# Performance work log

Hardware: AMD Instinct MI355X
Metric: run time of the kernel (lower is better)

Reference implementation:

```python
import jax, jax.numpy as jnp
import numpy as np

B, CIN, H, W = 4, 64, 160, 160
G, K = 8, 3
KK = K * K
PAD = K // 2
CG = CIN // G  # channels per deformable group


def setup_inputs() -> dict:
    key = jax.random.key(0)
    ks = jax.random.split(key, 6)
    x = jax.random.normal(ks[0], (B, CIN, H, W), jnp.float32)
    feat = jax.random.normal(ks[1], (B, CIN, H, W), jnp.float32)
    # conv_offset weights (zero-init in the original; small random here so offsets are nontrivial)
    w_off = jax.random.normal(ks[2], (3 * G * KK, CIN, 3, 3), jnp.float32) * 0.01
    b_off = jax.random.normal(ks[3], (3 * G * KK,), jnp.float32) * 0.01
    # deformable conv weights (torchvision DeformConv2d: groups=1, bias=True)
    w_dcn = jax.random.normal(ks[4], (CIN, CIN, K, K), jnp.float32) * (1.0 / np.sqrt(CIN * KK))
    b_dcn = jax.random.normal(ks[5], (CIN,), jnp.float32) * 0.01
    return dict(x=x, feat=feat, w_off=w_off, b_off=b_off, w_dcn=w_dcn, b_dcn=b_dcn)


def _modulated_deform_conv(x, offset, mask, w, b):
    # x: [B,C,H,W]; offset: [B,2*G*KK,H,W] (interleaved dy,dx per (g,k));
    # mask: [B,G*KK,H,W]; w: [Cout,C,K,K]; stride 1, zero padding K//2.
    Bn, C, Hh, Ww = x.shape
    off = offset.reshape(Bn, G, KK, 2, Hh, Ww)
    dy = off[:, :, :, 0]  # [B,G,KK,H,W]
    dx = off[:, :, :, 1]
    ki = jnp.arange(K)
    base_y = (jnp.repeat(ki, K) - PAD).reshape(1, 1, KK, 1, 1).astype(x.dtype)
    base_x = (jnp.tile(ki, K) - PAD).reshape(1, 1, KK, 1, 1).astype(x.dtype)
    hy = jnp.arange(Hh, dtype=x.dtype).reshape(1, 1, 1, Hh, 1)
    wx = jnp.arange(Ww, dtype=x.dtype).reshape(1, 1, 1, 1, Ww)
    py = hy + base_y + dy  # sample rows  [B,G,KK,H,W]
    px = wx + base_x + dx  # sample cols
    y0 = jnp.floor(py)
    x0 = jnp.floor(px)
    ly = py - y0
    lx = px - x0
    y0i = y0.astype(jnp.int32)
    x0i = x0.astype(jnp.int32)
    xg = x.reshape(Bn, G, CG, Hh * Ww)

    def gather(yi, xi):
        valid = ((yi >= 0) & (yi < Hh) & (xi >= 0) & (xi < Ww)).astype(x.dtype)
        idx = jnp.clip(yi, 0, Hh - 1) * Ww + jnp.clip(xi, 0, Ww - 1)
        flat = idx.reshape(Bn, G, 1, KK * Hh * Ww)
        v = jnp.take_along_axis(xg, flat, axis=3).reshape(Bn, G, CG, KK, Hh, Ww)
        return v * valid[:, :, None]  # zero padding outside

    v = ((1 - ly) * (1 - lx))[:, :, None] * gather(y0i, x0i) \
      + ((1 - ly) * lx)[:, :, None] * gather(y0i, x0i + 1) \
      + (ly * (1 - lx))[:, :, None] * gather(y0i + 1, x0i) \
      + (ly * lx)[:, :, None] * gather(y0i + 1, x0i + 1)
    v = v * mask.reshape(Bn, G, 1, KK, Hh, Ww)
    wr = w.reshape(w.shape[0], G, CG, KK)
    out = jnp.einsum('ogck,bgckhw->bohw', wr, v) + b[None, :, None, None]
    return out


def reference(x, feat, w_off, b_off, w_dcn, b_dcn):
    # conv_offset: 3x3 conv, stride 1, pad 1
    out = jax.lax.conv_general_dilated(
        feat, w_off, (1, 1), ((1, 1), (1, 1)),
        dimension_numbers=('NCHW', 'OIHW', 'NCHW')) + b_off[None, :, None, None]
    o1, o2, m = jnp.split(out, 3, axis=1)
    offset = jnp.concatenate([o1, o2], axis=1)  # [B, 2*G*KK, H, W]
    mask = jax.nn.sigmoid(m)                    # [B, G*KK, H, W]
    return _modulated_deform_conv(x, offset, mask, w_dcn, b_dcn)
```

## Files before the change

### kernel.cpp

```cpp
#include <hip/hip_runtime.h>
#include <math.h>

#define Bn   4
#define CINc 64
#define Hh   160
#define Ww   160
#define Gg   8
#define HW   (Hh * Ww)
#define COFF 216

#define VROW 200
#define SMEM_U32 7040
#define MASKL_OFF_U16 9344

typedef short bf16x8 __attribute__((ext_vector_type(8)));
typedef float f32x4  __attribute__((ext_vector_type(4)));

static __device__ __forceinline__ unsigned short f2bf(float f) {
    unsigned int u = __float_as_uint(f);
    u = (u + 0x7fffu + ((u >> 16) & 1u)) >> 16;
    return (unsigned short)u;
}
static __device__ __forceinline__ float bf2f(unsigned short s) {
    return __uint_as_float(((unsigned int)s) << 16);
}
static __device__ __forceinline__ float blo(unsigned int u) {
    return __uint_as_float(u << 16);
}
static __device__ __forceinline__ float bhi(unsigned int u) {
    return __uint_as_float(u & 0xffff0000u);
}

__global__ __launch_bounds__(256)
void prep_kernel(const float* __restrict__ feat, const float* __restrict__ x,
                 const float* __restrict__ w_off, const float* __restrict__ w_dcn,
                 unsigned short* __restrict__ featT, unsigned short* __restrict__ xG,
                 unsigned short* __restrict__ wofrag, unsigned short* __restrict__ wfrag) {
    const int blk = blockIdx.x;
    const int t = threadIdx.x;
    if (blk < 800) {
        const int b  = blk / 200;
        const int q  = (blk % 200) * 32 + (t >> 3);
        const int cj = t & 7;
        const float* fb = feat + (size_t)b * CINc * HW;
        float4 v[8];
        #pragma unroll
        for (int m = 0; m < 8; ++m)
            v[m] = *(const float4*)(fb + (size_t)(cj * 8 + m) * HW + q * 4);
        uint4* dst = (uint4*)featT + ((size_t)b * HW + q * 4) * 8 + cj;
        #pragma unroll
        for (int k = 0; k < 4; ++k) {
            float e[8];
            #pragma unroll
            for (int m = 0; m < 8; ++m) {
                const float4 vv = v[m];
                e[m] = (k == 0) ? vv.x : (k == 1) ? vv.y : (k == 2) ? vv.z : vv.w;
            }
            unsigned int d0, d1, d2, d3;
            asm("v_cvt_pk_bf16_f32 %0, %1, %2" : "=v"(d0) : "v"(e[0]), "v"(e[1]));
            asm("v_cvt_pk_bf16_f32 %0, %1, %2" : "=v"(d1) : "v"(e[2]), "v"(e[3]));
            asm("v_cvt_pk_bf16_f32 %0, %1, %2" : "=v"(d2) : "v"(e[4]), "v"(e[5]));
            asm("v_cvt_pk_bf16_f32 %0, %1, %2" : "=v"(d3) : "v"(e[6]), "v"(e[7]));
            uint4 r4; r4.x = d0; r4.y = d1; r4.z = d2; r4.w = d3;
            dst[(size_t)k * 8] = r4;
        }
    } else if (blk < 1600) {
        const int r  = blk - 800;
        const int bg = r / 25;
        const int q  = (r % 25) * 256 + t;
        const float* xb = x + ((size_t)(bg >> 3) * CINc + (size_t)(bg & 7) * 8) * HW;
        float4 v[8];
        #pragma unroll
        for (int cg = 0; cg < 8; ++cg)
            v[cg] = *(const float4*)(xb + (size_t)cg * HW + q * 4);
        uint4* dst = (uint4*)xG + (size_t)bg * HW + q * 4;
        #pragma unroll
        for (int k = 0; k < 4; ++k) {
            float e[8];
            #pragma unroll
            for (int cg = 0; cg < 8; ++cg) {
                const float4 vv = v[cg];
                e[cg] = (k == 0) ? vv.x : (k == 1) ? vv.y : (k == 2) ? vv.z : vv.w;
            }
            unsigned int d0, d1, d2, d3;
            asm("v_cvt_pk_bf16_f32 %0, %1, %2" : "=v"(d0) : "v"(e[0]), "v"(e[1]));
            asm("v_cvt_pk_bf16_f32 %0, %1, %2" : "=v"(d1) : "v"(e[2]), "v"(e[3]));
            asm("v_cvt_pk_bf16_f32 %0, %1, %2" : "=v"(d2) : "v"(e[4]), "v"(e[5]));
            asm("v_cvt_pk_bf16_f32 %0, %1, %2" : "=v"(d3) : "v"(e[6]), "v"(e[7]));
            uint4 r4; r4.x = d0; r4.y = d1; r4.z = d2; r4.w = d3;
            dst[k] = r4;
        }
    } else {
        for (int e = (blk - 1600) * 256 + t; e < 147456 + 36864; e += 180 * 256) {
            if (e < 147456) {
                const int j    = e & 7;
                const int lane = (e >> 3) & 63;
                const int rest = e >> 9;
                const int mt = rest & 15;
                const int q  = rest >> 4;
                const int ks = q & 1;
                const int kp = q >> 1;
                const int co = mt * 16 + (lane & 15);
                const int ci = ks * 32 + (lane >> 4) * 8 + j;
                float v = (co < COFF) ? w_off[(size_t)co * 576 + ci * 9 + kp] : 0.f;
                wofrag[e] = f2bf(v);
            } else {
                const int e2   = e - 147456;
                const int j    = e2 & 7;
                const int lane = (e2 >> 3) & 63;
                const int mt   = (e2 >> 9) & 3;
                const int ks   = e2 >> 11;
                const int m = mt * 16 + (lane & 15);
                const int k = ks * 32 + (lane >> 4) * 8 + j;
                const int g = k / 72, r = k % 72;
                const int kk = r >> 3, cg = r & 7;
                const int ci = g * 8 + cg;
                wfrag[e2] = f2bf(w_dcn[((size_t)m * CINc + ci) * 9 + kk]);
            }
        }
    }
}

#define BLEND_J(out_, w00, w01, w10, w11, c00, c01, c10, c11) {            \
    float vl_ = (c00) * blo(w00) + (c01) * blo(w01)                        \
              + (c10) * blo(w10) + (c11) * blo(w11);                       \
    float vh_ = (c00) * bhi(w00) + (c01) * bhi(w01)                        \
              + (c10) * bhi(w10) + (c11) * bhi(w11);                       \
    asm("v_cvt_pk_bf16_f32 %0, %1, %2" : "=v"(out_) : "v"(vl_), "v"(vh_)); \
}

__global__ __launch_bounds__(256, 4)
void dcnpack_fused(const unsigned short* __restrict__ featT,
                   const unsigned short* __restrict__ xG,
                   const unsigned short* __restrict__ wofrag,
                   const unsigned short* __restrict__ wfrag,
                   const float* __restrict__ b_off,
                   const float* __restrict__ b_dcn,
                   float* __restrict__ out) {
    __shared__ unsigned int smem4[SMEM_U32];
    unsigned short* halo   = (unsigned short*)smem4;
    unsigned int*   offsYX = smem4;
    unsigned short* maskL  = (unsigned short*)smem4 + MASKL_OFF_U16;
    unsigned short* vbuf   = (unsigned short*)smem4;

    const int b  = blockIdx.z;
    const int h0 = blockIdx.y * 8;
    const int w0 = blockIdx.x * 8;
    const int t  = threadIdx.x;
    const int wv   = t >> 6;
    const int lane = t & 63;
    const int n    = lane & 15;
    const int kg   = lane >> 4;

    for (int task = t; task < 800; task += 256) {
        const int pix = task >> 3, ch = task & 7;
        const int ry = pix / 10, rx = pix % 10;
        const int gh = h0 - 1 + ry, gw = w0 - 1 + rx;
        float4 v = make_float4(0.f, 0.f, 0.f, 0.f);
        if (gh >= 0 && gh < Hh && gw >= 0 && gw < Ww)
            v = *(const float4*)(featT + ((((size_t)b * Hh) + gh) * Ww + gw) * CINc + ch * 8);
        *(float4*)(halo + pix * 72 + ch * 8) = v;
    }
    __syncthreads();

    const int bbase0 = (((n >> 3) * 10) + (n & 7)) * 72 + kg * 8;

    f32x4 cacc[4][4] = {};
    bf16x8 af[3][4];
    #pragma unroll
    for (int i = 0; i < 4; ++i)
        af[0][i] = *(const bf16x8*)(wofrag + (((size_t)0 * 16 + wv + 4 * i) * 64 + lane) * 8);
    #pragma unroll
    for (int i = 0; i < 4; ++i)
        af[1][i] = *(const bf16x8*)(wofrag + (((size_t)1 * 16 + wv + 4 * i) * 64 + lane) * 8);

    #pragma unroll
    for (int s = 0; s < 18; ++s) {
        if (s + 2 < 18) {
            #pragma unroll
            for (int i = 0; i < 4; ++i)
                af[(s + 2) % 3][i] = *(const bf16x8*)(wofrag +
                    (((size_t)(s + 2) * 16 + wv + 4 * i) * 64 + lane) * 8);
        }
        const int kp = s >> 1, ks = s & 1;
        const int ky = kp / 3, kx = kp % 3;
        #pragma unroll
        for (int nt = 0; nt < 4; ++nt) {
            const bf16x8 bfr = *(const bf16x8*)(halo + bbase0 + nt * 1440 +
                                                (ky * 10 + kx) * 72 + ks * 32);
            #pragma unroll
            for (int i = 0; i < 4; ++i)
                cacc[i][nt] = __builtin_amdgcn_mfma_f32_16x16x32_bf16(af[s % 3][i], bfr, cacc[i][nt], 0, 0, 0);
        }
    }
    __syncthreads();

    #pragma unroll
    for (int i = 0; i < 4; ++i) {
        const int mt = wv + 4 * i;
        #pragma unroll
        for (int nt = 0; nt < 4; ++nt) {
            const int p = nt * 16 + n;
            if (mt < 9) {
                const int cob = mt * 16 + kg * 4;
                const int gkA = cob >> 1;
                const float v0 = cacc[i][nt][0] + b_off[cob + 0];
                const float v1 = cacc[i][nt][1] + b_off[cob + 1];
                const float v2 = cacc[i][nt][2] + b_off[cob + 2];
                const float v3 = cacc[i][nt][3] + b_off[cob + 3];
                unsigned int w01, w23;
                asm("v_cvt_pk_bf16_f32 %0, %1, %2" : "=v"(w01) : "v"(v0), "v"(v1));
                asm("v_cvt_pk_bf16_f32 %0, %1, %2" : "=v"(w23) : "v"(v2), "v"(v3));
                offsYX[p * 73 + gkA]     = w01;
                offsYX[p * 73 + gkA + 1] = w23;
            } else {
                #pragma unroll
                for (int r = 0; r < 4; ++r) {
                    const int co = mt * 16 + kg * 4 + r;
                    if (co < COFF) {
                        float v = cacc[i][nt][r] + b_off[co];
                        v = 1.f / (1.f + expf(-v));
                        maskL[p * 74 + (co - 144)] = f2bf(v);
                    }
                }
            }
        }
    }
    __syncthreads();

    const int p_t = t & 63;
    unsigned int yx[18];
    unsigned int mkp[9];
    #pragma unroll
    for (int c = 0; c < 3; ++c)
        #pragma unroll
        for (int it = 0; it < 6; ++it)
            yx[c * 6 + it] = offsYX[p_t * 73 + (c * 24 + wv + it * 4)];
    #pragma unroll
    for (int ii = 0; ii < 9; ++ii) {
        const int i0 = 2 * ii, i1 = 2 * ii + 1;
        const int u0 = (i0 / 6) * 24 + wv + (i0 % 6) * 4;
        const int u1 = (i1 / 6) * 24 + wv + (i1 % 6) * 4;
        const unsigned int m0 = maskL[p_t * 74 + u0];
        const unsigned int m1 = maskL[p_t * 74 + u1];
        mkp[ii] = m0 | (m1 << 16);
    }
    __syncthreads();

    f32x4 dacc[4] = {};
    const int h_s = h0 + (p_t >> 3);
    const int w_s = w0 + (p_t & 7);

    #pragma unroll
    for (int c = 0; c < 3; ++c) {
        float cf[6][4];
        uint4 q[6][4];
        #pragma unroll
        for (int it = 0; it < 6; ++it) {
            const int idx = c * 6 + it;
            const int u = c * 24 + wv + it * 4;
            const int g = u / 9;
            const int k = u % 9;

            const float dy   = blo(yx[idx]);
            const float dx   = bhi(yx[idx]);
            const float mask = (idx & 1) ? bhi(mkp[idx >> 1]) : blo(mkp[idx >> 1]);

            const float py  = (float)h_s + (float)(k / 3 - 1) + dy;
            const float pxx = (float)w_s + (float)(k % 3 - 1) + dx;
            const float y0f = floorf(py), x0f = floorf(pxx);
            const float ly = py - y0f, lx = pxx - x0f;
            const int y0 = (int)y0f, x0i = (int)x0f;
            const int y1 = y0 + 1,  x1  = x0i + 1;

            const float vy0 = (y0 >= 0 && y0 < Hh) ? 1.f : 0.f;
            const float vy1 = (y1 >= 0 && y1 < Hh) ? 1.f : 0.f;
            const float vx0 = (x0i >= 0 && x0i < Ww) ? 1.f : 0.f;
            const float vx1 = (x1 >= 0 && x1 < Ww) ? 1.f : 0.f;

            cf[it][0] = (1.f - ly) * (1.f - lx) * vy0 * vx0 * mask;
            cf[it][1] = (1.f - ly) * lx         * vy0 * vx1 * mask;
            cf[it][2] = ly         * (1.f - lx) * vy1 * vx0 * mask;
            cf[it][3] = ly         * lx         * vy1 * vx1 * mask;

            const int y0c = min(max(y0, 0), Hh - 1), y1c = min(max(y1, 0), Hh - 1);
            const int x0c = min(max(x0i, 0), Ww - 1), x1c = min(max(x1, 0), Ww - 1);

            const unsigned short* xb = xG + ((size_t)b * Gg + g) * HW * 8;
            q[it][0] = *(const uint4*)(xb + ((size_t)y0c * Ww + x0c) * 8);
            q[it][1] = *(const uint4*)(xb + ((size_t)y0c * Ww + x1c) * 8);
            q[it][2] = *(const uint4*)(xb + ((size_t)y1c * Ww + x0c) * 8);
            q[it][3] = *(const uint4*)(xb + ((size_t)y1c * Ww + x1c) * 8);
        }

        #pragma unroll
        for (int it = 0; it < 6; ++it) {
            unsigned int rr0, rr1, rr2, rr3;
            BLEND_J(rr0, q[it][0].x, q[it][1].x, q[it][2].x, q[it][3].x,
                    cf[it][0], cf[it][1], cf[it][2], cf[it][3]);
            BLEND_J(rr1, q[it][0].y, q[it][1].y, q[it][2].y, q[it][3].y,
                    cf[it][0], cf[it][1], cf[it][2], cf[it][3]);
            BLEND_J(rr2, q[it][0].z, q[it][1].z, q[it][2].z, q[it][3].z,
                    cf[it][0], cf[it][1], cf[it][2], cf[it][3]);
            BLEND_J(rr3, q[it][0].w, q[it][1].w, q[it][2].w, q[it][3].w,
                    cf[it][0], cf[it][1], cf[it][2], cf[it][3]);
            uint4 res; res.x = rr0; res.y = rr1; res.z = rr2; res.w = rr3;
            *(uint4*)(vbuf + (size_t)p_t * VROW + (wv + it * 4) * 8) = res;
        }

        bf16x8 afr[6];
        #pragma unroll
        for (int s = 0; s < 6; ++s)
            afr[s] = *(const bf16x8*)(wfrag + (((size_t)(c * 6 + s) * 4 + wv) * 64 + lane) * 8);

        __syncthreads();

        #pragma unroll
        for (int s = 0; s < 6; ++s) {
            #pragma unroll
            for (int nt = 0; nt < 4; ++nt) {
                const bf16x8 bfr = *(const bf16x8*)(vbuf + (nt * 16 + n) * VROW + s * 32 + kg * 8);
                dacc[nt] = __builtin_amdgcn_mfma_f32_16x16x32_bf16(afr[s], bfr, dacc[nt], 0, 0, 0);
            }
        }
        __syncthreads();
    }

    #pragma unroll
    for (int nt = 0; nt < 4; ++nt) {
        const int p = nt * 16 + n;
        const int h = h0 + (p >> 3);
        const int w = w0 + (p & 7);
        #pragma unroll
        for (int r = 0; r < 4; ++r) {
            const int o = wv * 16 + kg * 4 + r;
            out[(((size_t)b * CINc + o) * HW) + h * Ww + w] = dacc[nt][r] + b_dcn[o];
        }
    }
}

extern "C" void kernel_launch(void* const* d_in, const int* in_sizes, int n_in,
                              void* d_out, int out_size, void* d_ws, size_t ws_size,
                              hipStream_t stream) {
    const float* x     = (const float*)d_in[0];
    const float* feat  = (const float*)d_in[1];
    const float* w_off = (const float*)d_in[2];
    const float* b_off = (const float*)d_in[3];
    const float* w_dcn = (const float*)d_in[4];
    const float* b_dcn = (const float*)d_in[5];
    float* out = (float*)d_out;

    unsigned short* featT  = (unsigned short*)d_ws;
    unsigned short* xG     = featT + (size_t)Bn * HW * CINc;
    unsigned short* wofrag = xG + (size_t)Bn * HW * CINc;
    unsigned short* wfrag  = wofrag + (size_t)147456;

    prep_kernel<<<dim3(1780), 256, 0, stream>>>(
        feat, x, w_off, w_dcn, featT, xG, wofrag, wfrag);
    dcnpack_fused<<<dim3(Ww / 8, Hh / 8, Bn), 256, 0, stream>>>(
        featT, xG, wofrag, wfrag, b_off, b_dcn, out);
}
```

Before: 220.8 us.

## Split deform sampling into six smaller windows with separate vbuf region

The sampling/MFMA loop now runs over six windows of 12 (group,tap) units instead of three windows of 24. This halves per-iteration register arrays (gather results, coefficients, weight fragments). Offsets and masks are read directly from LDS each iteration instead of being preloaded into registers. The value buffer moves to its own LDS region, growing shared memory to 40KB, which removes one barrier. The intent is lower register pressure, at the cost of more barriers per block, more LDS use and less memory-level parallelism per window.

Measured after the change: 233.7 us. +5.8%, slower.

```diff
diff --git a/kernel.cpp b/kernel.cpp
--- a/kernel.cpp
+++ b/kernel.cpp
@@ -6,12 +6,16 @@
 #define Hh   160
 #define Ww   160
 #define Gg   8
-#define HW   (Hh * Ww)
+#define HW   (Hh * 160)
 #define COFF 216
 
-#define VROW 200
-#define SMEM_U32 7040
+#define NWIN 6
+#define WU   12
+#define VROW 100
+
+#define SMEM_U32 10240
 #define MASKL_OFF_U16 9344
+#define VBUF_OFF_U16  14080
 
 typedef short bf16x8 __attribute__((ext_vector_type(8)));
 typedef float f32x4  __attribute__((ext_vector_type(4)));
@@ -141,7 +145,7 @@
     unsigned short* halo   = (unsigned short*)smem4;
     unsigned int*   offsYX = smem4;
     unsigned short* maskL  = (unsigned short*)smem4 + MASKL_OFF_U16;
-    unsigned short* vbuf   = (unsigned short*)smem4;
+    unsigned short* vbuf   = (unsigned short*)smem4 + VBUF_OFF_U16;
 
     const int b  = blockIdx.z;
     const int h0 = blockIdx.y * 8;
@@ -228,43 +232,24 @@
     }
     __syncthreads();
 
+    f32x4 dacc[4] = {};
     const int p_t = t & 63;
-    unsigned int yx[18];
-    unsigned int mkp[9];
-    #pragma unroll
-    for (int c = 0; c < 3; ++c)
-        #pragma unroll
-        for (int it = 0; it < 6; ++it)
-            yx[c * 6 + it] = offsYX[p_t * 73 + (c * 24 + wv + it * 4)];
-    #pragma unroll
-    for (int ii = 0; ii < 9; ++ii) {
-        const int i0 = 2 * ii, i1 = 2 * ii + 1;
-        const int u0 = (i0 / 6) * 24 + wv + (i0 % 6) * 4;
-        const int u1 = (i1 / 6) * 24 + wv + (i1 % 6) * 4;
-        const unsigned int m0 = maskL[p_t * 74 + u0];
-        const unsigned int m1 = maskL[p_t * 74 + u1];
-        mkp[ii] = m0 | (m1 << 16);
-    }
-    __syncthreads();
-
-    f32x4 dacc[4] = {};
     const int h_s = h0 + (p_t >> 3);
     const int w_s = w0 + (p_t & 7);
 
-    #pragma unroll
-    for (int c = 0; c < 3; ++c) {
-        float cf[6][4];
-        uint4 q[6][4];
-        #pragma unroll
-        for (int it = 0; it < 6; ++it) {
-            const int idx = c * 6 + it;
-            const int u = c * 24 + wv + it * 4;
+    for (int c = 0; c < NWIN; ++c) {
+        float cf[3][4];
+        uint4 q[3][4];
+        #pragma unroll
+        for (int it = 0; it < 3; ++it) {
+            const int u = c * WU + wv + it * 4;
             const int g = u / 9;
             const int k = u % 9;
 
-            const float dy   = blo(yx[idx]);
-            const float dx   = bhi(yx[idx]);
-            const float mask = (idx & 1) ? bhi(mkp[idx >> 1]) : blo(mkp[idx >> 1]);
+            const unsigned int yx = offsYX[p_t * 73 + u];
+            const float dy   = blo(yx);
+            const float dx   = bhi(yx);
+            const float mask = bf2f(maskL[p_t * 74 + u]);
 
             const float py  = (float)h_s + (float)(k / 3 - 1) + dy;
             const float pxx = (float)w_s + (float)(k % 3 - 1) + dx;
@@ -294,7 +279,7 @@
         }
 
         #pragma unroll
-        for (int it = 0; it < 6; ++it) {
+        for (int it = 0; it < 3; ++it) {
             unsigned int rr0, rr1, rr2, rr3;
             BLEND_J(rr0, q[it][0].x, q[it][1].x, q[it][2].x, q[it][3].x,
                     cf[it][0], cf[it][1], cf[it][2], cf[it][3]);
@@ -308,15 +293,15 @@
             *(uint4*)(vbuf + (size_t)p_t * VROW + (wv + it * 4) * 8) = res;
         }
 
-        bf16x8 afr[6];
-        #pragma unroll
-        for (int s = 0; s < 6; ++s)
-            afr[s] = *(const bf16x8*)(wfrag + (((size_t)(c * 6 + s) * 4 + wv) * 64 + lane) * 8);
+        bf16x8 afr[3];
+        #pragma unroll
+        for (int s = 0; s < 3; ++s)
+            afr[s] = *(const bf16x8*)(wfrag + (((size_t)(c * 3 + s) * 4 + wv) * 64 + lane) * 8);
 
         __syncthreads();
 
         #pragma unroll
-        for (int s = 0; s < 6; ++s) {
+        for (int s = 0; s < 3; ++s) {
             #pragma unroll
             for (int nt = 0; nt < 4; ++nt) {
                 const bf16x8 bfr = *(const bf16x8*)(vbuf + (nt * 16 + n) * VROW + s * 32 + kg * 8);
```
